# Kernel tuning notes

Hardware: AMD Instinct MI355X
Metric: run time of the kernel (lower is better)

The kernel has to match this reference:

```python
import jax, jax.numpy as jnp
import numpy as np

B, N, E, H = 2, 2048, 1024, 16
D = E // H  # head dim = 64


def setup_inputs() -> dict:
    key = jax.random.key(0)
    ks = jax.random.split(key, 5)
    s = 0.02
    return {
        "x": jax.random.normal(ks[0], (B, N, E), dtype=jnp.float32),
        "w_qkv": jax.random.normal(ks[1], (3 * E, E), dtype=jnp.float32) * s,
        "b_qkv": jax.random.normal(ks[2], (3 * E,), dtype=jnp.float32) * s,
        "w_proj": jax.random.normal(ks[3], (E, E), dtype=jnp.float32) * s,
        "b_proj": jax.random.normal(ks[4], (E,), dtype=jnp.float32) * s,
    }


def reference(x, w_qkv, b_qkv, w_proj, b_proj):
    # qkv projection: [B, N, 3E]
    qkv = x @ w_qkv.T + b_qkv
    # einops 'b n (h d qkv) -> qkv b h n d': qkv index is INNERMOST in the split
    qkv = qkv.reshape(B, N, H, D, 3)
    qkv = jnp.transpose(qkv, (4, 0, 2, 1, 3))  # [3, B, H, N, D]
    q, k, v = qkv[0], qkv[1], qkv[2]
    scale = 1.0 / jnp.sqrt(jnp.asarray(D, dtype=x.dtype))
    att = jnp.einsum('bhnd,bhmd->bhnm', q, k) * scale  # [B, H, N, N]
    att = jax.nn.softmax(att, axis=-1)
    out = jnp.einsum('bhnm,bhmd->bhnd', att, v)  # [B, H, N, D]
    out = jnp.transpose(out, (0, 2, 1, 3)).reshape(B, N, E)  # b n (h d)
    return out @ w_proj.T + b_proj
```

## Files before the change

kernel.cpp:

```cpp
#include <hip/hip_runtime.h>
#include <hip/hip_bf16.h>
#include <math.h>

#define B_   2
#define N_   2048
#define E_   1024
#define H_   16
#define D_   64
#define E3_  3072
#define M_   (B_ * N_)

#define QSCALE 0.18033688011112042f

using short8 = __attribute__((ext_vector_type(8))) short;
using f32x4  = __attribute__((ext_vector_type(4))) float;
using uint2v = __attribute__((ext_vector_type(2))) unsigned int;

#define MFMA16(a, b, c) __builtin_amdgcn_mfma_f32_16x16x32_bf16((a), (b), (c), 0, 0, 0)

__device__ __forceinline__ unsigned short f2bf(float f) {
    __hip_bfloat16 h = __float2bfloat16(f);
    return __builtin_bit_cast(unsigned short, h);
}

__device__ __forceinline__ float fast_exp2(float x) {
#if __has_builtin(__builtin_amdgcn_exp2f)
    return __builtin_amdgcn_exp2f(x);
#else
    return exp2f(x);
#endif
}

__device__ __forceinline__ unsigned int pack_bf16_rh(float lo, float hi) {
    unsigned int ulo = __builtin_bit_cast(unsigned int, lo) + 0x8000u;
    unsigned int uhi = __builtin_bit_cast(unsigned int, hi) + 0x8000u;
#if __has_builtin(__builtin_amdgcn_perm)
    return __builtin_amdgcn_perm(uhi, ulo, 0x07060302u);
#else
    return (uhi & 0xFFFF0000u) | (ulo >> 16);
#endif
}

__device__ __forceinline__ void gl16(const void* g, void* l) {
    __builtin_amdgcn_global_load_lds(
        (__attribute__((address_space(1))) const void*)g,
        (__attribute__((address_space(3))) void*)l, 16, 0, 0);
}

__global__ __launch_bounds__(256) void convert_kernel(
    const float* __restrict__ x, const float* __restrict__ wq,
    const float* __restrict__ wp, const float* __restrict__ b_qkv,
    unsigned short* __restrict__ xb, unsigned short* __restrict__ wqp,
    unsigned short* __restrict__ wpb, float* __restrict__ bias_perm)
{
    if (blockIdx.x == 4096) {
        for (int q = threadIdx.x; q < E3_; q += 256) {
            const int c = q >> 10, rem = q & 1023;
            const int h = rem >> 6, d = rem & 63;
            float v = b_qkv[h * 192 + d * 3 + c];
            if (c == 0) v *= QSCALE;
            bias_perm[q] = v;
        }
        return;
    }
    const int o = (blockIdx.x * 256 + threadIdx.x) * 8;
    const float* src;
    unsigned short* dst;
    if (o < 4194304) {
        src = x + o; dst = xb + o;
    } else if (o < 7340032) {
        const int oo = o - 4194304;
        const int s = oo >> 10, k = oo & 1023;
        const int c = s >> 10, rem = s & 1023;
        const int h = rem >> 6, d = rem & 63;
        src = wq + (size_t)(h * 192 + d * 3 + c) * E_ + k;
        dst = wqp + oo;
    } else {
        const int oo = o - 7340032;
        src = wp + oo; dst = wpb + oo;
    }
    float4 a = *(const float4*)src;
    float4 b = *(const float4*)(src + 4);
    uint2v p0, p1;
    p0.x = pack_bf16_rh(a.x, a.y); p0.y = pack_bf16_rh(a.z, a.w);
    p1.x = pack_bf16_rh(b.x, b.y); p1.y = pack_bf16_rh(b.z, b.w);
    *(uint2v*)dst = p0;
    *(uint2v*)(dst + 4) = p1;
}

#define GEMM_STAGE(dstA, dstB, Aglob, Bglob, k0)                             \
    {                                                                        \
        _Pragma("unroll")                                                    \
        for (int i2 = 0; i2 < 2; ++i2) {                                     \
            const int chunk = wv * 128 + i2 * 64 + lane;                     \
            const int row = chunk >> 2;                                      \
            const int gcg = (chunk & 3) ^ ((row >> 1) & 3);                  \
            const int lbase = (wv * 128 + i2 * 64) * 8;                      \
            gl16(Aglob + (size_t)(bm + row) * E_ + (k0) + gcg * 8,           \
                 &dstA[lbase]);                                              \
            gl16(Bglob + (size_t)(bn + row) * E_ + (k0) + gcg * 8,           \
                 &dstB[lbase]);                                              \
        }                                                                    \
    }

#define GEMM_COMPUTE(MARR, NARR)                                             \
    {                                                                        \
        const int sw = (l15 >> 1) & 3;                                       \
        short8 af[4], bf[4];                                                 \
        _Pragma("unroll")                                                    \
        for (int i = 0; i < 4; ++i) {                                        \
            const int ra = wr * 64 + i * 16 + l15;                           \
            const int rb = wc * 64 + i * 16 + l15;                           \
            af[i] = *(const short8*)&MARR[ra * 32 + ((quad ^ sw) * 8)];      \
            bf[i] = *(const short8*)&NARR[rb * 32 + ((quad ^ sw) * 8)];      \
        }                                                                    \
        _Pragma("unroll")                                                    \
        for (int i = 0; i < 4; ++i)                                          \
            _Pragma("unroll")                                                \
            for (int j = 0; j < 4; ++j)                                      \
                acc[i][j] = MFMA16(af[i], bf[j], acc[i][j]);                 \
    }

#define GEMM_PROLOG                                                          \
    const int t    = threadIdx.x;                                            \
    const int wv   = t >> 6, lane = t & 63;                                  \
    const int quad = lane >> 4, l15 = lane & 15;                             \
    const int wr   = wv & 1, wc = wv >> 1;                                   \
    f32x4 acc[4][4];                                                         \
    _Pragma("unroll")                                                        \
    for (int i = 0; i < 4; ++i)                                              \
        _Pragma("unroll")                                                    \
        for (int j = 0; j < 4; ++j) acc[i][j] = (f32x4){0.f, 0.f, 0.f, 0.f};

__global__ __launch_bounds__(256) void qkv_kernel(
    const unsigned short* __restrict__ A, const unsigned short* __restrict__ Bm,
    const float* __restrict__ bias_perm,
    unsigned short* __restrict__ Q, unsigned short* __restrict__ K,
    unsigned short* __restrict__ VT)
{
    __shared__ __attribute__((aligned(16))) unsigned short As[2][128 * 32];
    __shared__ __attribute__((aligned(16))) unsigned short Bs[2][128 * 32];
    GEMM_PROLOG
    const int bm = blockIdx.y * 128;
    const int bn = blockIdx.x * 128;
    const int c  = bn >> 10;

    GEMM_STAGE(As[0], Bs[0], A, Bm, 0);
    if (c < 2) {
        for (int it = 0; it < 32; ++it) {
            const int cur = it & 1;
            __syncthreads();
            if (it < 31)
                GEMM_STAGE(As[cur ^ 1], Bs[cur ^ 1], A, Bm, (it + 1) * 32);
            GEMM_COMPUTE(Bs[cur], As[cur]);
        }
        const float scale = (c == 0) ? QSCALE : 1.0f;
        unsigned short* dst0 = (c == 0) ? Q : K;
#pragma unroll
        for (int i = 0; i < 4; ++i) {
            const int s0 = bn + wr * 64 + i * 16 + quad * 4;
            const int h  = (s0 >> 6) & 15;
            const int d0 = s0 & 63;
            const float4 bq = *(const float4*)(bias_perm + s0);
#pragma unroll
            for (int j = 0; j < 4; ++j) {
                const int row = bm + wc * 64 + j * 16 + l15;
                const int b   = row >> 11, n = row & (N_ - 1);
                const float v0 = fmaf(acc[i][j][0], scale, bq.x);
                const float v1 = fmaf(acc[i][j][1], scale, bq.y);
                const float v2 = fmaf(acc[i][j][2], scale, bq.z);
                const float v3 = fmaf(acc[i][j][3], scale, bq.w);
                uint2v pk;
                pk.x = pack_bf16_rh(v0, v1);
                pk.y = pack_bf16_rh(v2, v3);
                *(uint2v*)(dst0 + (((size_t)b * H_ + h) * N_ + n) * D_ + d0) = pk;
            }
        }
    } else {
        for (int it = 0; it < 32; ++it) {
            const int cur = it & 1;
            __syncthreads();
            if (it < 31)
                GEMM_STAGE(As[cur ^ 1], Bs[cur ^ 1], A, Bm, (it + 1) * 32);
            GEMM_COMPUTE(As[cur], Bs[cur]);
        }
#pragma unroll
        for (int j = 0; j < 4; ++j) {
            const int s = bn + wc * 64 + j * 16 + l15;
            const int h = (s >> 6) & 15, d = s & 63;
            const float bv = bias_perm[s];
#pragma unroll
            for (int i = 0; i < 4; ++i) {
                const int row0 = bm + wr * 64 + i * 16 + quad * 4;
                const int b    = row0 >> 11, n0 = row0 & (N_ - 1);
                uint2v pk;
                pk.x = pack_bf16_rh(acc[i][j][0] + bv, acc[i][j][1] + bv);
                pk.y = pack_bf16_rh(acc[i][j][2] + bv, acc[i][j][3] + bv);
                *(uint2v*)(VT + (((size_t)b * H_ + h) * D_ + d) * N_ + n0) = pk;
            }
        }
    }
}

__global__ __launch_bounds__(256, 4) void attn_kernel(
    const unsigned short* __restrict__ Q, const unsigned short* __restrict__ K,
    const unsigned short* __restrict__ VT, unsigned short* __restrict__ CTX)
{
    __shared__ __attribute__((aligned(16))) unsigned short Ks[2][64 * 64];
    __shared__ __attribute__((aligned(16))) unsigned short Vs[2][64 * 64];
    __shared__ __attribute__((aligned(16))) unsigned short Ps[4][16 * 64];

    const int t    = threadIdx.x;
    const int wv   = t >> 6, lane = t & 63;
    const int quad = lane >> 4, l15 = lane & 15;
    const int qt   = blockIdx.x & 31;
    const int bh   = blockIdx.x >> 5;

    const unsigned short* Kp = K + (size_t)bh * N_ * D_;
    const unsigned short* Vp = VT + (size_t)bh * D_ * N_;
    const unsigned short* Qp = Q + ((size_t)bh * N_ + qt * 64 + wv * 16 + l15) * D_;

    const short8 qf0 = *(const short8*)(Qp + quad * 8);
    const short8 qf1 = *(const short8*)(Qp + 32 + quad * 8);

    const int koff0 = (quad ^ (l15 & 7)) * 8;
    const int koff1 = ((4 + quad) ^ (l15 & 7)) * 8;

    f32x4 O[4];
#pragma unroll
    for (int i = 0; i < 4; ++i) O[i] = (f32x4){0.f, 0.f, 0.f, 0.f};
    f32x4 lsum4 = {0.f, 0.f, 0.f, 0.f};

#define ATTN_STAGE(buf, kt)                                                  \
    {                                                                        \
        _Pragma("unroll")                                                    \
        for (int i2 = 0; i2 < 2; ++i2) {                                     \
            const int cch = (wv * 2 + i2) * 64 + lane;                       \
            const int row = cch >> 3, sg = cch & 7;                          \
            const int gc  = (sg ^ (row & 7)) * 8;                            \
            gl16(Kp + (size_t)((kt) * 64 + row) * D_ + gc,                   \
                 &Ks[buf][(wv * 2 + i2) * 512]);                             \
            gl16(Vp + (size_t)row * N_ + (kt) * 64 + gc,                     \
                 &Vs[buf][(wv * 2 + i2) * 512]);                             \
        }                                                                    \
    }

    ATTN_STAGE(0, 0);

    for (int kt = 0; kt < 32; ++kt) {
        const int cur = kt & 1;
        __syncthreads();
        if (kt < 31) ATTN_STAGE(cur ^ 1, kt + 1);

        f32x4 st[4];
#pragma unroll
        for (int kb = 0; kb < 4; ++kb) st[kb] = (f32x4){0.f, 0.f, 0.f, 0.f};
#pragma unroll
        for (int kb = 0; kb < 4; ++kb) {
            const int krow = (kb * 16 + l15) * 64;
            const short8 kf0 = *(const short8*)&Ks[cur][krow + koff0];
            const short8 kf1 = *(const short8*)&Ks[cur][krow + koff1];
            st[kb] = MFMA16(kf0, qf0, st[kb]);
            st[kb] = MFMA16(kf1, qf1, st[kb]);
        }

#pragma unroll
        for (int kb = 0; kb < 4; ++kb) {
            f32x4 pv;
#pragma unroll
            for (int g = 0; g < 4; ++g) pv[g] = fast_exp2(st[kb][g]);
            lsum4 += pv;
            uint2v pk;
            pk.x = pack_bf16_rh(pv[0], pv[1]);
            pk.y = pack_bf16_rh(pv[2], pv[3]);
            const int pgrp = kb * 2 + (quad >> 1);
            const int poff = ((pgrp ^ (l15 & 7)) * 8) + (quad & 1) * 4;
            *(uint2v*)&Ps[wv][l15 * 64 + poff] = pk;
        }

#pragma unroll
        for (int ks = 0; ks < 2; ++ks) {
            const int pslot = ((ks * 4 + quad) ^ (l15 & 7)) * 8;
            const short8 pf = *(const short8*)&Ps[wv][l15 * 64 + pslot];
            const int koff = ks ? koff1 : koff0;
#pragma unroll
            for (int nt = 0; nt < 4; ++nt) {
                const short8 vf =
                    *(const short8*)&Vs[cur][(nt * 16 + l15) * 64 + koff];
                O[nt] = MFMA16(pf, vf, O[nt]);
            }
        }
    }

    float lt = lsum4[0] + lsum4[1] + lsum4[2] + lsum4[3];
    lt += __shfl_xor(lt, 16, 64);
    lt += __shfl_xor(lt, 32, 64);

    const int b = bh >> 4, h = bh & 15;
#pragma unroll
    for (int g = 0; g < 4; ++g) {
        const float lg  = __shfl(lt, quad * 4 + g, 64);
        const float inv = 1.0f / lg;
        const int qrow  = qt * 64 + wv * 16 + quad * 4 + g;
#pragma unroll
        for (int nt = 0; nt < 4; ++nt)
            CTX[((size_t)b * N_ + qrow) * E_ + h * D_ + nt * 16 + l15] =
                f2bf(O[nt][g] * inv);
    }
#undef ATTN_STAGE
}

__global__ __launch_bounds__(256) void proj_kernel(
    const unsigned short* __restrict__ A, const unsigned short* __restrict__ Bm,
    const float* __restrict__ bias, float* __restrict__ out)
{
    __shared__ __attribute__((aligned(16))) unsigned short As[2][128 * 32];
    __shared__ __attribute__((aligned(16))) unsigned short Bs[2][128 * 32];
    GEMM_PROLOG
    const int bm = blockIdx.y * 128;
    const int bn = blockIdx.x * 128;

    GEMM_STAGE(As[0], Bs[0], A, Bm, 0);
    for (int it = 0; it < 32; ++it) {
        const int cur = it & 1;
        __syncthreads();
        if (it < 31)
            GEMM_STAGE(As[cur ^ 1], Bs[cur ^ 1], A, Bm, (it + 1) * 32);
        GEMM_COMPUTE(Bs[cur], As[cur]);
    }

#pragma unroll
    for (int i = 0; i < 4; ++i) {
        const int col0 = bn + wr * 64 + i * 16 + quad * 4;
        const float4 bp = *(const float4*)(bias + col0);
#pragma unroll
        for (int j = 0; j < 4; ++j) {
            const int row = bm + wc * 64 + j * 16 + l15;
            float4 o;
            o.x = acc[i][j][0] + bp.x;
            o.y = acc[i][j][1] + bp.y;
            o.z = acc[i][j][2] + bp.z;
            o.w = acc[i][j][3] + bp.w;
            *(float4*)(out + (size_t)row * E_ + col0) = o;
        }
    }
}

extern "C" void kernel_launch(void* const* d_in, const int* in_sizes, int n_in,
                              void* d_out, int out_size, void* d_ws, size_t ws_size,
                              hipStream_t stream)
{
    const float* x      = (const float*)d_in[0];
    const float* w_qkv  = (const float*)d_in[1];
    const float* b_qkv  = (const float*)d_in[2];
    const float* w_proj = (const float*)d_in[3];
    const float* b_proj = (const float*)d_in[4];
    float* out = (float*)d_out;

    unsigned short* xb  = (unsigned short*)d_ws;
    unsigned short* wqp = xb  + 4194304;
    unsigned short* wpb = wqp + 3145728;
    unsigned short* Q   = wpb + 1048576;
    unsigned short* K   = Q   + 4194304;
    unsigned short* VT  = K   + 4194304;
    unsigned short* CTX = VT  + 4194304;
    float* bias_perm    = (float*)(CTX + 4194304);

    dim3 blk(256);
    convert_kernel<<<dim3(4097), blk, 0, stream>>>(
        x, w_qkv, w_proj, b_qkv, xb, wqp, wpb, bias_perm);

    qkv_kernel<<<dim3(24, 32), blk, 0, stream>>>(xb, wqp, bias_perm, Q, K, VT);

    attn_kernel<<<dim3(B_ * H_ * (N_ / 64)), blk, 0, stream>>>(Q, K, VT, CTX);

    proj_kernel<<<dim3(8, 32), blk, 0, stream>>>(CTX, wpb, b_proj, out);
}
```

Before: 208.5 us.

## Split attention key tiles across waves and reduce partial outputs in LDS

Each wave in the attention kernel now handles all 64 query rows against its own 16-key slice of every K/V tile, instead of 16 query rows against all 64 keys. The score accumulator feeds the PV MFMA directly as a 16x16x16 operand, so the per-wave P round-trip through LDS goes away. At the end, partial O and row sums from the four waves are reduced through LDS before normalisation. The cost is four times more O accumulator registers (occupancy hint lowered from 4 to 3), half-width PV MFMAs, and an extra cross-wave reduction phase with more barriers.

```diff
diff --git a/kernel.cpp b/kernel.cpp
--- a/kernel.cpp
+++ b/kernel.cpp
@@ -12,11 +12,13 @@
 
 #define QSCALE 0.18033688011112042f
 
-using short8 = __attribute__((ext_vector_type(8))) short;
-using f32x4  = __attribute__((ext_vector_type(4))) float;
-using uint2v = __attribute__((ext_vector_type(2))) unsigned int;
-
-#define MFMA16(a, b, c) __builtin_amdgcn_mfma_f32_16x16x32_bf16((a), (b), (c), 0, 0, 0)
+using short8  = __attribute__((ext_vector_type(8))) short;
+using short4v = __attribute__((ext_vector_type(4))) short;
+using f32x4   = __attribute__((ext_vector_type(4))) float;
+using uint2v  = __attribute__((ext_vector_type(2))) unsigned int;
+
+#define MFMA16(a, b, c)   __builtin_amdgcn_mfma_f32_16x16x32_bf16((a), (b), (c), 0, 0, 0)
+#define MFMA16K16(a, b, c) __builtin_amdgcn_mfma_f32_16x16x16bf16_1k((a), (b), (c), 0, 0, 0)
 
 __device__ __forceinline__ unsigned short f2bf(float f) {
     __hip_bfloat16 h = __float2bfloat16(f);
@@ -39,6 +41,13 @@
 #else
     return (uhi & 0xFFFF0000u) | (ulo >> 16);
 #endif
+}
+
+__device__ __forceinline__ short4v pack4_bf16(float a, float b, float c, float d) {
+    uint2v u;
+    u.x = pack_bf16_rh(a, b);
+    u.y = pack_bf16_rh(c, d);
+    return __builtin_bit_cast(short4v, u);
 }
 
 __device__ __forceinline__ void gl16(const void* g, void* l) {
@@ -202,13 +211,12 @@
     }
 }
 
-__global__ __launch_bounds__(256, 4) void attn_kernel(
+__global__ __launch_bounds__(256, 3) void attn_kernel(
     const unsigned short* __restrict__ Q, const unsigned short* __restrict__ K,
     const unsigned short* __restrict__ VT, unsigned short* __restrict__ CTX)
 {
-    __shared__ __attribute__((aligned(16))) unsigned short Ks[2][64 * 64];
-    __shared__ __attribute__((aligned(16))) unsigned short Vs[2][64 * 64];
-    __shared__ __attribute__((aligned(16))) unsigned short Ps[4][16 * 64];
+    __shared__ __attribute__((aligned(16))) unsigned short pool[16384];
+    __shared__ float lsumBuf[4][64];
 
     const int t    = threadIdx.x;
     const int wv   = t >> 6, lane = t & 63;
@@ -218,18 +226,26 @@
 
     const unsigned short* Kp = K + (size_t)bh * N_ * D_;
     const unsigned short* Vp = VT + (size_t)bh * D_ * N_;
-    const unsigned short* Qp = Q + ((size_t)bh * N_ + qt * 64 + wv * 16 + l15) * D_;
-
-    const short8 qf0 = *(const short8*)(Qp + quad * 8);
-    const short8 qf1 = *(const short8*)(Qp + 32 + quad * 8);
+
+    short8 qf[4][2];
+#pragma unroll
+    for (int s = 0; s < 4; ++s) {
+        const unsigned short* Qp =
+            Q + ((size_t)bh * N_ + qt * 64 + s * 16 + l15) * D_;
+        qf[s][0] = *(const short8*)(Qp + quad * 8);
+        qf[s][1] = *(const short8*)(Qp + 32 + quad * 8);
+    }
 
     const int koff0 = (quad ^ (l15 & 7)) * 8;
     const int koff1 = ((4 + quad) ^ (l15 & 7)) * 8;
-
-    f32x4 O[4];
-#pragma unroll
-    for (int i = 0; i < 4; ++i) O[i] = (f32x4){0.f, 0.f, 0.f, 0.f};
-    f32x4 lsum4 = {0.f, 0.f, 0.f, 0.f};
+    const int vslot = (((wv * 2 + (quad >> 1)) ^ (l15 & 7)) * 8) + (quad & 1) * 4;
+
+    f32x4 O[4][4];
+#pragma unroll
+    for (int s = 0; s < 4; ++s)
+#pragma unroll
+        for (int nt = 0; nt < 4; ++nt) O[s][nt] = (f32x4){0.f, 0.f, 0.f, 0.f};
+    float lsums[4] = {0.f, 0.f, 0.f, 0.f};
 
 #define ATTN_STAGE(buf, kt)                                                  \
     {                                                                        \
@@ -239,9 +255,9 @@
             const int row = cch >> 3, sg = cch & 7;                          \
             const int gc  = (sg ^ (row & 7)) * 8;                            \
             gl16(Kp + (size_t)((kt) * 64 + row) * D_ + gc,                   \
-                 &Ks[buf][(wv * 2 + i2) * 512]);                             \
+                 &pool[(buf) * 4096 + (wv * 2 + i2) * 512]);                 \
             gl16(Vp + (size_t)row * N_ + (kt) * 64 + gc,                     \
-                 &Vs[buf][(wv * 2 + i2) * 512]);                             \
+                 &pool[8192 + (buf) * 4096 + (wv * 2 + i2) * 512]);          \
         }                                                                    \
     }
 
@@ -252,62 +268,106 @@
         __syncthreads();
         if (kt < 31) ATTN_STAGE(cur ^ 1, kt + 1);
 
+        const unsigned short* Kc = pool + cur * 4096;
+        const unsigned short* Vc = pool + 8192 + cur * 4096;
+
+        const int krow = (wv * 16 + l15) * 64;
+        const short8 kf0 = *(const short8*)&Kc[krow + koff0];
+        const short8 kf1 = *(const short8*)&Kc[krow + koff1];
+
         f32x4 st[4];
 #pragma unroll
-        for (int kb = 0; kb < 4; ++kb) st[kb] = (f32x4){0.f, 0.f, 0.f, 0.f};
-#pragma unroll
-        for (int kb = 0; kb < 4; ++kb) {
-            const int krow = (kb * 16 + l15) * 64;
-            const short8 kf0 = *(const short8*)&Ks[cur][krow + koff0];
-            const short8 kf1 = *(const short8*)&Ks[cur][krow + koff1];
-            st[kb] = MFMA16(kf0, qf0, st[kb]);
-            st[kb] = MFMA16(kf1, qf1, st[kb]);
-        }
-
-#pragma unroll
-        for (int kb = 0; kb < 4; ++kb) {
-            f32x4 pv;
-#pragma unroll
-            for (int g = 0; g < 4; ++g) pv[g] = fast_exp2(st[kb][g]);
-            lsum4 += pv;
-            uint2v pk;
-            pk.x = pack_bf16_rh(pv[0], pv[1]);
-            pk.y = pack_bf16_rh(pv[2], pv[3]);
-            const int pgrp = kb * 2 + (quad >> 1);
-            const int poff = ((pgrp ^ (l15 & 7)) * 8) + (quad & 1) * 4;
-            *(uint2v*)&Ps[wv][l15 * 64 + poff] = pk;
-        }
-
-#pragma unroll
-        for (int ks = 0; ks < 2; ++ks) {
-            const int pslot = ((ks * 4 + quad) ^ (l15 & 7)) * 8;
-            const short8 pf = *(const short8*)&Ps[wv][l15 * 64 + pslot];
-            const int koff = ks ? koff1 : koff0;
+        for (int s = 0; s < 4; ++s) st[s] = (f32x4){0.f, 0.f, 0.f, 0.f};
+#pragma unroll
+        for (int s = 0; s < 4; ++s) st[s] = MFMA16(kf0, qf[s][0], st[s]);
+#pragma unroll
+        for (int s = 0; s < 4; ++s) st[s] = MFMA16(kf1, qf[s][1], st[s]);
+
+        short4v pa[4];
+#pragma unroll
+        for (int s = 0; s < 4; ++s) {
+            float p0 = fast_exp2(st[s][0]);
+            float p1 = fast_exp2(st[s][1]);
+            float p2 = fast_exp2(st[s][2]);
+            float p3 = fast_exp2(st[s][3]);
+            lsums[s] += (p0 + p1) + (p2 + p3);
+            pa[s] = pack4_bf16(p0, p1, p2, p3);
+        }
+
+        short4v bv[4];
+#pragma unroll
+        for (int nt = 0; nt < 4; ++nt)
+            bv[nt] = *(const short4v*)&Vc[(nt * 16 + l15) * 64 + vslot];
+#pragma unroll
+        for (int s = 0; s < 4; ++s)
+#pragma unroll
+            for (int nt = 0; nt < 4; ++nt)
+                O[s][nt] = MFMA16K16(pa[s], bv[nt], O[s][nt]);
+    }
+#undef ATTN_STAGE
+
+#pragma unroll
+    for (int s = 0; s < 4; ++s) {
+        lsums[s] += __shfl_xor(lsums[s], 16, 64);
+        lsums[s] += __shfl_xor(lsums[s], 32, 64);
+    }
+    if (quad == 0) {
+#pragma unroll
+        for (int s = 0; s < 4; ++s) lsumBuf[wv][s * 16 + l15] = lsums[s];
+    }
+    __syncthreads();
+
+    float* red = (float*)pool;
+    const int b = bh >> 4, h = bh & 15;
+
+#pragma unroll
+    for (int r = 0; r < 2; ++r) {
+#pragma unroll
+        for (int so = 0; so < 2; ++so) {
+            const int s = 2 * r + so;
+            if (wv != s) {
+                float* dst = red + so * 4096 + wv * 1024;
+#pragma unroll
+                for (int nt = 0; nt < 4; ++nt)
+#pragma unroll
+                    for (int g = 0; g < 4; ++g)
+                        dst[(quad * 4 + g) * 64 + nt * 16 + l15] = O[s][nt][g];
+            }
+        }
+        __syncthreads();
+        if ((wv >> 1) == r) {
+            const int s = wv;
+            const int so = s & 1;
+            float ltot[4];
+#pragma unroll
+            for (int g = 0; g < 4; ++g) {
+                float lv = 0.f;
+#pragma unroll
+                for (int w = 0; w < 4; ++w)
+                    lv += lsumBuf[w][s * 16 + quad * 4 + g];
+                ltot[g] = 1.0f / lv;
+            }
 #pragma unroll
             for (int nt = 0; nt < 4; ++nt) {
-                const short8 vf =
-                    *(const short8*)&Vs[cur][(nt * 16 + l15) * 64 + koff];
-                O[nt] = MFMA16(pf, vf, O[nt]);
+                f32x4 o = O[s][nt];
+#pragma unroll
+                for (int w = 0; w < 4; ++w) {
+                    if (w == s) continue;
+#pragma unroll
+                    for (int g = 0; g < 4; ++g)
+                        o[g] += red[so * 4096 + w * 1024 +
+                                    (quad * 4 + g) * 64 + nt * 16 + l15];
+                }
+#pragma unroll
+                for (int g = 0; g < 4; ++g) {
+                    const int qrow = qt * 64 + s * 16 + quad * 4 + g;
+                    CTX[((size_t)b * N_ + qrow) * E_ + h * D_ + nt * 16 + l15] =
+                        f2bf(o[g] * ltot[g]);
+                }
             }
         }
-    }
-
-    float lt = lsum4[0] + lsum4[1] + lsum4[2] + lsum4[3];
-    lt += __shfl_xor(lt, 16, 64);
-    lt += __shfl_xor(lt, 32, 64);
-
-    const int b = bh >> 4, h = bh & 15;
-#pragma unroll
-    for (int g = 0; g < 4; ++g) {
-        const float lg  = __shfl(lt, quad * 4 + g, 64);
-        const float inv = 1.0f / lg;
-        const int qrow  = qt * 64 + wv * 16 + quad * 4 + g;
-#pragma unroll
-        for (int nt = 0; nt < 4; ++nt)
-            CTX[((size_t)b * N_ + qrow) * E_ + h * D_ + nt * 16 + l15] =
-                f2bf(O[nt][g] * inv);
-    }
-#undef ATTN_STAGE
+        __syncthreads();
+    }
 }
 
 __global__ __launch_bounds__(256) void proj_kernel(
```

Measured after the change: 453.1 us. 2.17x slower.
